# Kernel tuning notes

Hardware: AMD Instinct MI355X
Metric: run time of the kernel (lower is better)

Reference implementation:

```python
import jax, jax.numpy as jnp
import numpy as np

E = 16        # n_experts
K = 2         # n_active_experts
D = 2048      # d_model
F = 1408      # ffn_hidden
B, S = 4, 2048


def _swiglu(x, wg, wu, wd):
    # x: [N, D]; wg/wu: [F, D]; wd: [D, F]
    return (jax.nn.silu(x @ wg.T) * (x @ wu.T)) @ wd.T


def setup_inputs() -> dict:
    key = jax.random.key(0)
    ks = jax.random.split(key, 8)
    sc = 0.02
    return {
        "x": jax.random.normal(ks[0], (B, S, D), jnp.float32),
        "gate_w": jax.random.normal(ks[1], (E, D), jnp.float32) * sc,
        "w_gate": jax.random.normal(ks[2], (E, F, D), jnp.float32) * sc,
        "w_up": jax.random.normal(ks[3], (E, F, D), jnp.float32) * sc,
        "w_down": jax.random.normal(ks[4], (E, D, F), jnp.float32) * sc,
        "sw_gate": jax.random.normal(ks[5], (F, D), jnp.float32) * sc,
        "sw_up": jax.random.normal(ks[6], (F, D), jnp.float32) * sc,
        "sw_down": jax.random.normal(ks[7], (D, F), jnp.float32) * sc,
        "expert_bias": jnp.zeros((E,), jnp.float32),
    }


def reference(x, gate_w, w_gate, w_up, w_down, sw_gate, sw_up, sw_down, expert_bias):
    b, s, d = x.shape
    flat = x.reshape(-1, d)                           # [N, D]
    logits = flat @ gate_w.T                          # [N, E]
    probs = jax.nn.softmax(logits, axis=-1)
    biased = logits + expert_bias
    _, top_idx = jax.lax.top_k(biased, K)             # [N, K] int32
    top_w = jnp.take_along_axis(probs, top_idx, axis=-1)
    top_w = top_w / jnp.sum(top_w, axis=-1, keepdims=True)
    # scatter top-k weights into a dense per-expert combine matrix [N, E]
    combine = jnp.sum(jax.nn.one_hot(top_idx, E, dtype=flat.dtype) * top_w[..., None], axis=1)
    out = jnp.zeros_like(flat)
    for e in range(E):  # fixed small expert loop
        out = out + combine[:, e:e + 1] * _swiglu(flat, w_gate[e], w_up[e], w_down[e])
    out = out + _swiglu(flat, sw_gate, sw_up, sw_down)  # shared expert
    return out.reshape(b, s, d)
```

## Files before the change

kernel.cpp:

```cpp
#include <hip/hip_runtime.h>
#include <hip/hip_bf16.h>
#include <cstdint>

#define NE 16
#define D_ 2048
#define F_ 1408
#define NTOK 8192
#define NPAIR (NTOK * 2)
#define SHARED_BASE NPAIR
#define NTOT (NPAIR + NTOK)

#define BM1 256
#define BN1 128
#define BK 64
#define NF1 (F_ / BN1)
#define NF2 (D_ / BN1)
#define MAXRT1 111
#define MAXRT2 79

typedef __attribute__((ext_vector_type(8))) short short8;
typedef __attribute__((ext_vector_type(4))) float f32x4;

static __device__ __forceinline__ ushort f2bf(float f) {
    union { float f; unsigned u; } v; v.f = f;
    unsigned u = v.u;
    return (ushort)((u + 0x7FFFu + ((u >> 16) & 1u)) >> 16);
}

static __device__ __forceinline__ void cvt_store8(ushort* dst, const float* src) {
    const float4* s = reinterpret_cast<const float4*>(src);
    float4 a = s[0], b = s[1];
    short8 v;
    v[0] = (short)f2bf(a.x); v[1] = (short)f2bf(a.y);
    v[2] = (short)f2bf(a.z); v[3] = (short)f2bf(a.w);
    v[4] = (short)f2bf(b.x); v[5] = (short)f2bf(b.y);
    v[6] = (short)f2bf(b.z); v[7] = (short)f2bf(b.w);
    *reinterpret_cast<short8*>(dst) = v;
}

static __device__ __forceinline__ void gll16(const void* g, void* l) {
    __builtin_amdgcn_global_load_lds((const __attribute__((address_space(1))) void*)g,
                                     (__attribute__((address_space(3))) void*)l, 16, 0, 0);
}

__global__ __launch_bounds__(256) void k_cvt(const float* __restrict__ src,
                                             ushort* __restrict__ dst, int n8) {
    int i = blockIdx.x * 256 + threadIdx.x;
    int stride = gridDim.x * 256;
    for (; i < n8; i += stride) cvt_store8(dst + (size_t)i * 8, src + (size_t)i * 8);
}

__global__ __launch_bounds__(256) void k_route(const float* __restrict__ x,
                                               const float* __restrict__ gate_w,
                                               const float* __restrict__ expert_bias,
                                               int* __restrict__ topk_idx,
                                               float* __restrict__ topk_w) {
    const int wave = threadIdx.x >> 6;
    const int lane = threadIdx.x & 63;
    const int tok = blockIdx.x * 4 + wave;
    if (tok >= NTOK) return;
    const float* xr = x + (size_t)tok * D_;
    float xv[D_ / 64];
#pragma unroll
    for (int i = 0; i < D_ / 64; ++i) xv[i] = xr[lane + 64 * i];

    float logits[NE];
#pragma unroll
    for (int e = 0; e < NE; ++e) {
        const float* gw = gate_w + e * D_;
        float p = 0.f;
#pragma unroll
        for (int i = 0; i < D_ / 64; ++i) p += xv[i] * gw[lane + 64 * i];
#pragma unroll
        for (int off = 32; off > 0; off >>= 1) p += __shfl_xor(p, off, 64);
        logits[e] = p;
    }
    int i1 = 0; float b1 = logits[0] + expert_bias[0];
#pragma unroll
    for (int e = 1; e < NE; ++e) {
        float b = logits[e] + expert_bias[e];
        if (b > b1) { b1 = b; i1 = e; }
    }
    int i2 = -1; float b2 = -3.4e38f;
#pragma unroll
    for (int e = 0; e < NE; ++e) {
        if (e == i1) continue;
        float b = logits[e] + expert_bias[e];
        if (b > b2) { b2 = b; i2 = e; }
    }
    float l1 = logits[i1], l2 = logits[i2];
    float m = fmaxf(l1, l2);
    float e1 = __expf(l1 - m), e2 = __expf(l2 - m);
    float s = e1 + e2;
    if (lane == 0) {
        topk_idx[tok * 2 + 0] = i1;
        topk_idx[tok * 2 + 1] = i2;
        topk_w[tok * 2 + 0] = e1 / s;
        topk_w[tok * 2 + 1] = e2 / s;
    }
}

__global__ void k_zero_meta(int* meta) {
    if (threadIdx.x < 128) meta[threadIdx.x] = 0;
}

__global__ __launch_bounds__(256) void k_count(const int* __restrict__ topk_idx,
                                               int* __restrict__ meta) {
    int t = blockIdx.x * 256 + threadIdx.x;
    if (t >= NTOK) return;
    atomicAdd(&meta[topk_idx[t * 2 + 0]], 1);
    atomicAdd(&meta[topk_idx[t * 2 + 1]], 1);
}

__global__ void k_prefix(int* meta) {
    if (threadIdx.x == 0) {
        int acc = 0;
        for (int e = 0; e < NE; ++e) { meta[32 + e] = acc; acc += meta[e]; }
        meta[32 + NE] = acc;
        int t = 0;
        for (int e = 0; e < NE; ++e) { meta[64 + e] = t; t += (meta[e] + BM1 - 1) / BM1; }
        meta[64 + NE] = t;
        meta[64 + NE + 1] = t + NTOK / BM1;
    }
}

__global__ __launch_bounds__(256) void k_scatter(const int* __restrict__ topk_idx,
                                                 const float* __restrict__ topk_w,
                                                 int* __restrict__ meta,
                                                 int* __restrict__ tok_sorted,
                                                 float* __restrict__ w_sorted) {
    int t = blockIdx.x * 256 + threadIdx.x;
    if (t >= NTOK) return;
#pragma unroll
    for (int k = 0; k < 2; ++k) {
        int e = topk_idx[t * 2 + k];
        int p = atomicAdd(&meta[16 + e], 1);
        int idx = meta[32 + e] + p;
        tok_sorted[idx] = t;
        w_sorted[idx] = topk_w[t * 2 + k];
    }
}

__global__ __launch_bounds__(512, 2) void k_ffn1(const ushort* __restrict__ xb,
                                                 const ushort* __restrict__ wgb,
                                                 const ushort* __restrict__ wub,
                                                 const ushort* __restrict__ swgb,
                                                 const ushort* __restrict__ swub,
                                                 const int* __restrict__ meta,
                                                 const int* __restrict__ tok_sorted,
                                                 const float* __restrict__ w_sorted,
                                                 ushort* __restrict__ Hbuf) {
    const int bid = blockIdx.x;
    const int rt = bid / NF1;
    const int fx = bid - rt * NF1;
    if (rt >= meta[64 + NE + 1]) return;
    int e = (rt >= meta[64 + NE]) ? NE : 0;
    if (e == 0) {
#pragma unroll
        for (int i = 1; i < NE; ++i) if (rt >= meta[64 + i]) e = i;
    }
    int n_e, base;
    if (e < NE) { n_e = meta[e]; base = meta[32 + e]; }
    else        { n_e = NTOK;    base = SHARED_BASE; }
    const int row0 = (rt - meta[64 + e]) * BM1;
    const int f0 = fx * BN1;
    const ushort* wg = (e < NE) ? wgb + (size_t)e * F_ * D_ : swgb;
    const ushort* wu = (e < NE) ? wub + (size_t)e * F_ * D_ : swub;

    __shared__ __align__(16) ushort As[2][BM1 * BK];
    __shared__ __align__(16) ushort Gs[2][BN1 * BK];
    __shared__ __align__(16) ushort Us[2][BN1 * BK];
    __shared__ int tks[BM1];
    __shared__ float tws[BM1];

    const int tid = threadIdx.x;
    const int wv = tid >> 6, lane = tid & 63;
    if (tid < BM1) {
        int r = row0 + tid;
        if (r < n_e) {
            tks[tid] = (e < NE) ? tok_sorted[base + r] : r;
            tws[tid] = (e < NE) ? w_sorted[base + r] : 1.0f;
        } else { tks[tid] = 0; tws[tid] = 0.f; }
    }
    __syncthreads();

    const ushort* srcA[4]; const ushort* srcG[2]; const ushort* srcU[2];
#pragma unroll
    for (int j = 0; j < 4; ++j) {
        int c = j * 512 + wv * 64 + lane;
        int r = c >> 3;
        int col = ((c & 7) ^ (r & 7)) * 8;
        srcA[j] = xb + (size_t)tks[r] * D_ + col;
    }
#pragma unroll
    for (int j = 0; j < 2; ++j) {
        int c = j * 512 + wv * 64 + lane;
        int r = c >> 3;
        int col = ((c & 7) ^ (r & 7)) * 8;
        srcG[j] = wg + (size_t)(f0 + r) * D_ + col;
        srcU[j] = wu + (size_t)(f0 + r) * D_ + col;
    }

    auto stage = [&](int buf, int k0) {
        char* bA = (char*)(&As[buf][0]) + wv * 1024;
        char* bG = (char*)(&Gs[buf][0]) + wv * 1024;
        char* bU = (char*)(&Us[buf][0]) + wv * 1024;
        gll16(srcA[0] + k0, bA);         gll16(srcA[1] + k0, bA + 8192);
        gll16(srcA[2] + k0, bA + 16384); gll16(srcA[3] + k0, bA + 24576);
        gll16(srcG[0] + k0, bG);         gll16(srcG[1] + k0, bG + 8192);
        gll16(srcU[0] + k0, bU);         gll16(srcU[1] + k0, bU + 8192);
    };

    f32x4 accg[4][4] = {}; f32x4 accu[4][4] = {};
    const int wm = (wv >> 1) * 64, wn = (wv & 1) * 64;
    const int fr = lane & 15, fq = lane >> 4;
    const int sw = fr & 7;
    const int rc0 = ((fq ^ sw) * 8);
    const int rc1 = (((4 + fq) ^ sw) * 8);

    auto compute = [&](int buf) {
        const ushort* pA = As[buf];
        const ushort* pG = Gs[buf];
        const ushort* pU = Us[buf];
#pragma unroll
        for (int kk = 0; kk < 2; ++kk) {
            const int rc = kk ? rc1 : rc0;
            short8 af[4], gf[4], uf[4];
#pragma unroll
            for (int mi = 0; mi < 4; ++mi)
                af[mi] = *reinterpret_cast<const short8*>(&pA[(wm + mi * 16 + fr) * BK + rc]);
#pragma unroll
            for (int ni = 0; ni < 4; ++ni) {
                gf[ni] = *reinterpret_cast<const short8*>(&pG[(wn + ni * 16 + fr) * BK + rc]);
                uf[ni] = *reinterpret_cast<const short8*>(&pU[(wn + ni * 16 + fr) * BK + rc]);
            }
#pragma unroll
            for (int mi = 0; mi < 4; ++mi)
#pragma unroll
                for (int ni = 0; ni < 4; ++ni) {
                    accg[mi][ni] = __builtin_amdgcn_mfma_f32_16x16x32_bf16(af[mi], gf[ni], accg[mi][ni], 0, 0, 0);
                    accu[mi][ni] = __builtin_amdgcn_mfma_f32_16x16x32_bf16(af[mi], uf[ni], accu[mi][ni], 0, 0, 0);
                }
        }
    };

    const int NK = D_ / BK;
    stage(0, 0);
    stage(1, BK);
    asm volatile("s_waitcnt vmcnt(8)" ::: "memory");
    __builtin_amdgcn_s_barrier();
    __builtin_amdgcn_sched_barrier(0);
    int cur = 0;
    for (int ks = 0; ks < NK; ++ks) {
        compute(cur);
        __builtin_amdgcn_s_barrier();
        if (ks + 2 < NK) {
            stage(cur, (ks + 2) * BK);
            asm volatile("s_waitcnt vmcnt(8)" ::: "memory");
        } else if (ks + 1 < NK) {
            asm volatile("s_waitcnt vmcnt(0)" ::: "memory");
        }
        __builtin_amdgcn_s_barrier();
        __builtin_amdgcn_sched_barrier(0);
        cur ^= 1;
    }

#pragma unroll
    for (int mi = 0; mi < 4; ++mi) {
#pragma unroll
        for (int r = 0; r < 4; ++r) {
            int lr = wm + mi * 16 + fq * 4 + r;
            int grow = row0 + lr;
            if (grow < n_e) {
                float w = tws[lr];
                ushort* hrow = Hbuf + (size_t)(base + grow) * F_ + f0 + wn;
#pragma unroll
                for (int ni = 0; ni < 4; ++ni) {
                    float g = accg[mi][ni][r];
                    float u = accu[mi][ni][r];
                    float h = w * (g / (1.f + __expf(-g))) * u;
                    hrow[ni * 16 + fr] = f2bf(h);
                }
            }
        }
    }
}

__global__ __launch_bounds__(512, 2) void k_ffn2(const ushort* __restrict__ Hbuf,
                                                 const ushort* __restrict__ wdb,
                                                 const ushort* __restrict__ swdb,
                                                 const int* __restrict__ meta,
                                                 const int* __restrict__ tok_sorted,
                                                 float* __restrict__ out,
                                                 int shared_pass) {
    const int bid = blockIdx.x;
    const int rt = bid / NF2;
    const int dx = bid - rt * NF2;
    int e, n_e, base, row0;
    if (shared_pass) {
        e = NE; n_e = NTOK; base = SHARED_BASE; row0 = rt * BM1;
    } else {
        if (rt >= meta[64 + NE]) return;
        e = 0;
#pragma unroll
        for (int i = 1; i < NE; ++i) if (rt >= meta[64 + i]) e = i;
        n_e = meta[e]; base = meta[32 + e];
        row0 = (rt - meta[64 + e]) * BM1;
    }
    const int d0 = dx * BN1;
    const ushort* wd = (e < NE) ? wdb + (size_t)e * D_ * F_ : swdb;

    __shared__ __align__(16) ushort As[2][BM1 * BK];
    __shared__ __align__(16) ushort Bs[2][BN1 * BK];
    __shared__ int tks[BM1];

    const int tid = threadIdx.x;
    const int wv = tid >> 6, lane = tid & 63;
    if (tid < BM1) {
        int r = row0 + tid;
        tks[tid] = (r < n_e) ? ((e < NE) ? tok_sorted[base + r] : r) : -1;
    }
    __syncthreads();

    const ushort* srcA[4]; const ushort* srcB[2];
#pragma unroll
    for (int j = 0; j < 4; ++j) {
        int c = j * 512 + wv * 64 + lane;
        int r = c >> 3;
        int col = ((c & 7) ^ (r & 7)) * 8;
        srcA[j] = Hbuf + (size_t)(base + row0 + r) * F_ + col;
    }
#pragma unroll
    for (int j = 0; j < 2; ++j) {
        int c = j * 512 + wv * 64 + lane;
        int r = c >> 3;
        int col = ((c & 7) ^ (r & 7)) * 8;
        srcB[j] = wd + (size_t)(d0 + r) * F_ + col;
    }

    auto stage = [&](int buf, int k0) {
        char* bA = (char*)(&As[buf][0]) + wv * 1024;
        char* bB = (char*)(&Bs[buf][0]) + wv * 1024;
        gll16(srcA[0] + k0, bA);         gll16(srcA[1] + k0, bA + 8192);
        gll16(srcA[2] + k0, bA + 16384); gll16(srcA[3] + k0, bA + 24576);
        gll16(srcB[0] + k0, bB);         gll16(srcB[1] + k0, bB + 8192);
    };

    f32x4 acc[4][4] = {};
    const int wm = (wv >> 1) * 64, wn = (wv & 1) * 64;
    const int fr = lane & 15, fq = lane >> 4;
    const int sw = fr & 7;
    const int rc0 = ((fq ^ sw) * 8);
    const int rc1 = (((4 + fq) ^ sw) * 8);

    auto compute = [&](int buf) {
        const ushort* pA = As[buf];
        const ushort* pB = Bs[buf];
#pragma unroll
        for (int kk = 0; kk < 2; ++kk) {
            const int rc = kk ? rc1 : rc0;
            short8 af[4], bfr[4];
#pragma unroll
            for (int mi = 0; mi < 4; ++mi)
                af[mi] = *reinterpret_cast<const short8*>(&pA[(wm + mi * 16 + fr) * BK + rc]);
#pragma unroll
            for (int ni = 0; ni < 4; ++ni)
                bfr[ni] = *reinterpret_cast<const short8*>(&pB[(wn + ni * 16 + fr) * BK + rc]);
#pragma unroll
            for (int mi = 0; mi < 4; ++mi)
#pragma unroll
                for (int ni = 0; ni < 4; ++ni)
                    acc[mi][ni] = __builtin_amdgcn_mfma_f32_16x16x32_bf16(af[mi], bfr[ni], acc[mi][ni], 0, 0, 0);
        }
    };

    const int NK = F_ / BK;
    stage(0, 0);
    stage(1, BK);
    asm volatile("s_waitcnt vmcnt(6)" ::: "memory");
    __builtin_amdgcn_s_barrier();
    __builtin_amdgcn_sched_barrier(0);
    int cur = 0;
    for (int ks = 0; ks < NK; ++ks) {
        compute(cur);
        __builtin_amdgcn_s_barrier();
        if (ks + 2 < NK) {
            stage(cur, (ks + 2) * BK);
            asm volatile("s_waitcnt vmcnt(6)" ::: "memory");
        } else if (ks + 1 < NK) {
            asm volatile("s_waitcnt vmcnt(0)" ::: "memory");
        }
        __builtin_amdgcn_s_barrier();
        __builtin_amdgcn_sched_barrier(0);
        cur ^= 1;
    }

#pragma unroll
    for (int mi = 0; mi < 4; ++mi) {
#pragma unroll
        for (int r = 0; r < 4; ++r) {
            int lr = wm + mi * 16 + fq * 4 + r;
            int slot = row0 + lr;
            if (slot < n_e) {
                int t = tks[lr];
                float* orow = out + (size_t)t * D_ + d0 + wn;
#pragma unroll
                for (int ni = 0; ni < 4; ++ni) {
                    float val = acc[mi][ni][r];
                    if (shared_pass) orow[ni * 16 + fr] = val;
                    else atomicAdd(&orow[ni * 16 + fr], val);
                }
            }
        }
    }
}

extern "C" void kernel_launch(void* const* d_in, const int* in_sizes, int n_in,
                              void* d_out, int out_size, void* d_ws, size_t ws_size,
                              hipStream_t stream) {
    const float* x        = (const float*)d_in[0];
    const float* gate_w   = (const float*)d_in[1];
    const float* w_gate   = (const float*)d_in[2];
    const float* w_up     = (const float*)d_in[3];
    const float* w_down   = (const float*)d_in[4];
    const float* sw_gate  = (const float*)d_in[5];
    const float* sw_up    = (const float*)d_in[6];
    const float* sw_down  = (const float*)d_in[7];
    const float* expert_bias = (const float*)d_in[8];
    float* out = (float*)d_out;

    const size_t NW = (size_t)NE * F_ * D_;
    const size_t NSW = (size_t)F_ * D_;
    const size_t NX = (size_t)NTOK * D_;

    char* ws = (char*)d_ws;
    size_t off = 0;
    ushort* xb   = (ushort*)(ws + off); off += NX * 2;
    ushort* wgb  = (ushort*)(ws + off); off += NW * 2;
    ushort* wub  = (ushort*)(ws + off); off += NW * 2;
    ushort* wdb  = (ushort*)(ws + off); off += NW * 2;
    ushort* swgb = (ushort*)(ws + off); off += NSW * 2;
    ushort* swub = (ushort*)(ws + off); off += NSW * 2;
    ushort* swdb = (ushort*)(ws + off); off += NSW * 2;
    ushort* Hbuf = (ushort*)(ws + off); off += (size_t)NTOT * F_ * 2;
    int* tok_sorted = (int*)(ws + off); off += NPAIR * sizeof(int);
    float* w_sorted = (float*)(ws + off); off += NPAIR * sizeof(float);
    int* topk_idx = (int*)(ws + off); off += NTOK * 2 * sizeof(int);
    float* topk_w = (float*)(ws + off); off += NTOK * 2 * sizeof(float);
    int* meta = (int*)(ws + off); off += 512;

    k_route<<<NTOK / 4, 256, 0, stream>>>(x, gate_w, expert_bias, topk_idx, topk_w);
    k_zero_meta<<<1, 128, 0, stream>>>(meta);
    k_count<<<NTOK / 256, 256, 0, stream>>>(topk_idx, meta);
    k_prefix<<<1, 1, 0, stream>>>(meta);
    k_scatter<<<NTOK / 256, 256, 0, stream>>>(topk_idx, topk_w, meta, tok_sorted, w_sorted);

    auto cvt = [&](const float* s, ushort* d, size_t n) {
        int n8 = (int)(n / 8);
        int blocks = (n8 + 255) / 256;
        if (blocks > 4096) blocks = 4096;
        k_cvt<<<blocks, 256, 0, stream>>>(s, d, n8);
    };
    cvt(x, xb, NX);
    cvt(w_gate, wgb, NW);
    cvt(w_up, wub, NW);
    cvt(w_down, wdb, NW);
    cvt(sw_gate, swgb, NSW);
    cvt(sw_up, swub, NSW);
    cvt(sw_down, swdb, NSW);

    k_ffn1<<<MAXRT1 * NF1, 512, 0, stream>>>(xb, wgb, wub, swgb, swub,
                                             meta, tok_sorted, w_sorted, Hbuf);

    k_ffn2<<<(NTOK / BM1) * NF2, 512, 0, stream>>>(Hbuf, wdb, swdb, meta, tok_sorted, out, 1);
    k_ffn2<<<MAXRT2 * NF2, 512, 0, stream>>>(Hbuf, wdb, swdb, meta, tok_sorted, out, 0);
}
```

Measured before the change: 974.5 us.

## Interleave LDS reads and MFMA phases with barriers and priority boosts in FFN GEMMs

Splits each K-step of both grouped GEMM kernels into alternating LDS-fragment-load and MFMA phases separated by workgroup barriers. MFMA phases run under raised wave priority (s_setprio), a ping-pong schedule meant to let waves overlap one another's memory and matrix work. In the first kernel the A/G prefetch for step k+2 now issues before the last up-projection MFMA block, so global loads overlap compute. The cost is many extra barriers per iteration, which could stall the waves. The vmcnt accounting also becomes fragile: the wait count is unchanged even though loads are now issued in two groups.

```diff
diff --git a/kernel.cpp b/kernel.cpp
--- a/kernel.cpp
+++ b/kernel.cpp
@@ -140,6 +140,8 @@
         w_sorted[idx] = topk_w[t * 2 + k];
     }
 }
+
+#define LD8(P, ROW, RC) (*reinterpret_cast<const short8*>(&(P)[(ROW) * BK + (RC)]))
 
 __global__ __launch_bounds__(512, 2) void k_ffn1(const ushort* __restrict__ xb,
                                                  const ushort* __restrict__ wgb,
@@ -201,13 +203,15 @@
         srcU[j] = wu + (size_t)(f0 + r) * D_ + col;
     }
 
-    auto stage = [&](int buf, int k0) {
+    auto stageAG = [&](int buf, int k0) {
         char* bA = (char*)(&As[buf][0]) + wv * 1024;
         char* bG = (char*)(&Gs[buf][0]) + wv * 1024;
-        char* bU = (char*)(&Us[buf][0]) + wv * 1024;
         gll16(srcA[0] + k0, bA);         gll16(srcA[1] + k0, bA + 8192);
         gll16(srcA[2] + k0, bA + 16384); gll16(srcA[3] + k0, bA + 24576);
         gll16(srcG[0] + k0, bG);         gll16(srcG[1] + k0, bG + 8192);
+    };
+    auto stageU = [&](int buf, int k0) {
+        char* bU = (char*)(&Us[buf][0]) + wv * 1024;
         gll16(srcU[0] + k0, bU);         gll16(srcU[1] + k0, bU + 8192);
     };
 
@@ -218,51 +222,83 @@
     const int rc0 = ((fq ^ sw) * 8);
     const int rc1 = (((4 + fq) ^ sw) * 8);
 
-    auto compute = [&](int buf) {
-        const ushort* pA = As[buf];
-        const ushort* pG = Gs[buf];
-        const ushort* pU = Us[buf];
-#pragma unroll
-        for (int kk = 0; kk < 2; ++kk) {
-            const int rc = kk ? rc1 : rc0;
-            short8 af[4], gf[4], uf[4];
-#pragma unroll
-            for (int mi = 0; mi < 4; ++mi)
-                af[mi] = *reinterpret_cast<const short8*>(&pA[(wm + mi * 16 + fr) * BK + rc]);
-#pragma unroll
-            for (int ni = 0; ni < 4; ++ni) {
-                gf[ni] = *reinterpret_cast<const short8*>(&pG[(wn + ni * 16 + fr) * BK + rc]);
-                uf[ni] = *reinterpret_cast<const short8*>(&pU[(wn + ni * 16 + fr) * BK + rc]);
-            }
-#pragma unroll
-            for (int mi = 0; mi < 4; ++mi)
-#pragma unroll
-                for (int ni = 0; ni < 4; ++ni) {
-                    accg[mi][ni] = __builtin_amdgcn_mfma_f32_16x16x32_bf16(af[mi], gf[ni], accg[mi][ni], 0, 0, 0);
-                    accu[mi][ni] = __builtin_amdgcn_mfma_f32_16x16x32_bf16(af[mi], uf[ni], accu[mi][ni], 0, 0, 0);
-                }
-        }
-    };
-
     const int NK = D_ / BK;
-    stage(0, 0);
-    stage(1, BK);
+    stageAG(0, 0); stageU(0, 0);
+    stageAG(1, BK); stageU(1, BK);
     asm volatile("s_waitcnt vmcnt(8)" ::: "memory");
     __builtin_amdgcn_s_barrier();
     __builtin_amdgcn_sched_barrier(0);
-    int cur = 0;
+
     for (int ks = 0; ks < NK; ++ks) {
-        compute(cur);
-        __builtin_amdgcn_s_barrier();
-        if (ks + 2 < NK) {
-            stage(cur, (ks + 2) * BK);
+        const int cur = ks & 1;
+        const ushort* pA = As[cur];
+        const ushort* pG = Gs[cur];
+        const ushort* pU = Us[cur];
+        const bool st = (ks + 2 < NK);
+        const int k2 = (ks + 2) * BK;
+        short8 af[4], gf[4], uf[4];
+
+#pragma unroll
+        for (int mi = 0; mi < 4; ++mi) af[mi] = LD8(pA, wm + mi * 16 + fr, rc0);
+#pragma unroll
+        for (int ni = 0; ni < 4; ++ni) gf[ni] = LD8(pG, wn + ni * 16 + fr, rc0);
+        __builtin_amdgcn_s_barrier();
+        __builtin_amdgcn_s_setprio(1);
+#pragma unroll
+        for (int mi = 0; mi < 4; ++mi)
+#pragma unroll
+            for (int ni = 0; ni < 4; ++ni)
+                accg[mi][ni] = __builtin_amdgcn_mfma_f32_16x16x32_bf16(af[mi], gf[ni], accg[mi][ni], 0, 0, 0);
+        __builtin_amdgcn_s_setprio(0);
+        __builtin_amdgcn_s_barrier();
+
+#pragma unroll
+        for (int ni = 0; ni < 4; ++ni) uf[ni] = LD8(pU, wn + ni * 16 + fr, rc0);
+        __builtin_amdgcn_s_barrier();
+        __builtin_amdgcn_s_setprio(1);
+#pragma unroll
+        for (int mi = 0; mi < 4; ++mi)
+#pragma unroll
+            for (int ni = 0; ni < 4; ++ni)
+                accu[mi][ni] = __builtin_amdgcn_mfma_f32_16x16x32_bf16(af[mi], uf[ni], accu[mi][ni], 0, 0, 0);
+        __builtin_amdgcn_s_setprio(0);
+        __builtin_amdgcn_s_barrier();
+
+#pragma unroll
+        for (int mi = 0; mi < 4; ++mi) af[mi] = LD8(pA, wm + mi * 16 + fr, rc1);
+#pragma unroll
+        for (int ni = 0; ni < 4; ++ni) gf[ni] = LD8(pG, wn + ni * 16 + fr, rc1);
+        __builtin_amdgcn_s_barrier();
+        __builtin_amdgcn_s_setprio(1);
+#pragma unroll
+        for (int mi = 0; mi < 4; ++mi)
+#pragma unroll
+            for (int ni = 0; ni < 4; ++ni)
+                accg[mi][ni] = __builtin_amdgcn_mfma_f32_16x16x32_bf16(af[mi], gf[ni], accg[mi][ni], 0, 0, 0);
+        __builtin_amdgcn_s_setprio(0);
+        __builtin_amdgcn_s_barrier();
+
+#pragma unroll
+        for (int ni = 0; ni < 4; ++ni) uf[ni] = LD8(pU, wn + ni * 16 + fr, rc1);
+        if (st) stageAG(cur, k2);
+        __builtin_amdgcn_s_barrier();
+        __builtin_amdgcn_s_setprio(1);
+#pragma unroll
+        for (int mi = 0; mi < 4; ++mi)
+#pragma unroll
+            for (int ni = 0; ni < 4; ++ni)
+                accu[mi][ni] = __builtin_amdgcn_mfma_f32_16x16x32_bf16(af[mi], uf[ni], accu[mi][ni], 0, 0, 0);
+        __builtin_amdgcn_s_setprio(0);
+        __builtin_amdgcn_s_barrier();
+
+        if (st) {
+            stageU(cur, k2);
             asm volatile("s_waitcnt vmcnt(8)" ::: "memory");
         } else if (ks + 1 < NK) {
             asm volatile("s_waitcnt vmcnt(0)" ::: "memory");
         }
         __builtin_amdgcn_s_barrier();
         __builtin_amdgcn_sched_barrier(0);
-        cur ^= 1;
     }
 
 #pragma unroll
@@ -353,38 +389,49 @@
     const int rc0 = ((fq ^ sw) * 8);
     const int rc1 = (((4 + fq) ^ sw) * 8);
 
-    auto compute = [&](int buf) {
-        const ushort* pA = As[buf];
-        const ushort* pB = Bs[buf];
-#pragma unroll
-        for (int kk = 0; kk < 2; ++kk) {
-            const int rc = kk ? rc1 : rc0;
-            short8 af[4], bfr[4];
-#pragma unroll
-            for (int mi = 0; mi < 4; ++mi)
-                af[mi] = *reinterpret_cast<const short8*>(&pA[(wm + mi * 16 + fr) * BK + rc]);
-#pragma unroll
-            for (int ni = 0; ni < 4; ++ni)
-                bfr[ni] = *reinterpret_cast<const short8*>(&pB[(wn + ni * 16 + fr) * BK + rc]);
-#pragma unroll
-            for (int mi = 0; mi < 4; ++mi)
-#pragma unroll
-                for (int ni = 0; ni < 4; ++ni)
-                    acc[mi][ni] = __builtin_amdgcn_mfma_f32_16x16x32_bf16(af[mi], bfr[ni], acc[mi][ni], 0, 0, 0);
-        }
-    };
-
     const int NK = F_ / BK;
     stage(0, 0);
     stage(1, BK);
     asm volatile("s_waitcnt vmcnt(6)" ::: "memory");
     __builtin_amdgcn_s_barrier();
     __builtin_amdgcn_sched_barrier(0);
-    int cur = 0;
+
     for (int ks = 0; ks < NK; ++ks) {
-        compute(cur);
-        __builtin_amdgcn_s_barrier();
-        if (ks + 2 < NK) {
+        const int cur = ks & 1;
+        const ushort* pA = As[cur];
+        const ushort* pB = Bs[cur];
+        const bool st = (ks + 2 < NK);
+        short8 af[4], bfr[4];
+
+#pragma unroll
+        for (int mi = 0; mi < 4; ++mi) af[mi] = LD8(pA, wm + mi * 16 + fr, rc0);
+#pragma unroll
+        for (int ni = 0; ni < 4; ++ni) bfr[ni] = LD8(pB, wn + ni * 16 + fr, rc0);
+        __builtin_amdgcn_s_barrier();
+        __builtin_amdgcn_s_setprio(1);
+#pragma unroll
+        for (int mi = 0; mi < 4; ++mi)
+#pragma unroll
+            for (int ni = 0; ni < 4; ++ni)
+                acc[mi][ni] = __builtin_amdgcn_mfma_f32_16x16x32_bf16(af[mi], bfr[ni], acc[mi][ni], 0, 0, 0);
+        __builtin_amdgcn_s_setprio(0);
+        __builtin_amdgcn_s_barrier();
+
+#pragma unroll
+        for (int mi = 0; mi < 4; ++mi) af[mi] = LD8(pA, wm + mi * 16 + fr, rc1);
+#pragma unroll
+        for (int ni = 0; ni < 4; ++ni) bfr[ni] = LD8(pB, wn + ni * 16 + fr, rc1);
+        __builtin_amdgcn_s_barrier();
+        __builtin_amdgcn_s_setprio(1);
+#pragma unroll
+        for (int mi = 0; mi < 4; ++mi)
+#pragma unroll
+            for (int ni = 0; ni < 4; ++ni)
+                acc[mi][ni] = __builtin_amdgcn_mfma_f32_16x16x32_bf16(af[mi], bfr[ni], acc[mi][ni], 0, 0, 0);
+        __builtin_amdgcn_s_setprio(0);
+        __builtin_amdgcn_s_barrier();
+
+        if (st) {
             stage(cur, (ks + 2) * BK);
             asm volatile("s_waitcnt vmcnt(6)" ::: "memory");
         } else if (ks + 1 < NK) {
@@ -392,7 +439,6 @@
         }
         __builtin_amdgcn_s_barrier();
         __builtin_amdgcn_sched_barrier(0);
-        cur ^= 1;
     }
 
 #pragma unroll
```

New measurement: 1.065 ms. 1.09x slower.

## Replace atomic scatter in down-projection with bf16 staging buffer and gather

Applied to the files above, without the earlier changes.

The down-projection now runs routed and shared tiles in a single launch. It writes per-slot bf16 results into a staging buffer that reuses the expert gate-weight workspace, instead of storing and atomically adding fp32 values into the output. A new gather kernel uses an inverse index from the scatter step to sum each token's two expert rows and its shared row into fp32 output. This removes fp32 atomics and the second launch. In exchange it adds an extra read and write pass and rounds partial results to bf16 before summation.

```diff
diff --git a/kernel.cpp b/kernel.cpp
--- a/kernel.cpp
+++ b/kernel.cpp
@@ -15,8 +15,7 @@
 #define BK 64
 #define NF1 (F_ / BN1)
 #define NF2 (D_ / BN1)
-#define MAXRT1 111
-#define MAXRT2 79
+#define MAXRT 111
 
 typedef __attribute__((ext_vector_type(8))) short short8;
 typedef __attribute__((ext_vector_type(4))) float f32x4;
@@ -25,6 +24,11 @@
     union { float f; unsigned u; } v; v.f = f;
     unsigned u = v.u;
     return (ushort)((u + 0x7FFFu + ((u >> 16) & 1u)) >> 16);
+}
+
+static __device__ __forceinline__ float bf2f(ushort u) {
+    union { unsigned u; float f; } v; v.u = ((unsigned)u) << 16;
+    return v.f;
 }
 
 static __device__ __forceinline__ void cvt_store8(ushort* dst, const float* src) {
@@ -128,7 +132,8 @@
                                                  const float* __restrict__ topk_w,
                                                  int* __restrict__ meta,
                                                  int* __restrict__ tok_sorted,
-                                                 float* __restrict__ w_sorted) {
+                                                 float* __restrict__ w_sorted,
+                                                 int* __restrict__ inv) {
     int t = blockIdx.x * 256 + threadIdx.x;
     if (t >= NTOK) return;
 #pragma unroll
@@ -138,6 +143,7 @@
         int idx = meta[32 + e] + p;
         tok_sorted[idx] = t;
         w_sorted[idx] = topk_w[t * 2 + k];
+        inv[t * 2 + k] = idx;
     }
 }
 
@@ -290,37 +296,28 @@
                                                  const ushort* __restrict__ wdb,
                                                  const ushort* __restrict__ swdb,
                                                  const int* __restrict__ meta,
-                                                 const int* __restrict__ tok_sorted,
-                                                 float* __restrict__ out,
-                                                 int shared_pass) {
+                                                 ushort* __restrict__ Obuf) {
     const int bid = blockIdx.x;
     const int rt = bid / NF2;
     const int dx = bid - rt * NF2;
-    int e, n_e, base, row0;
-    if (shared_pass) {
-        e = NE; n_e = NTOK; base = SHARED_BASE; row0 = rt * BM1;
-    } else {
-        if (rt >= meta[64 + NE]) return;
-        e = 0;
+    if (rt >= meta[64 + NE + 1]) return;
+    int e = (rt >= meta[64 + NE]) ? NE : 0;
+    if (e == 0) {
 #pragma unroll
         for (int i = 1; i < NE; ++i) if (rt >= meta[64 + i]) e = i;
-        n_e = meta[e]; base = meta[32 + e];
-        row0 = (rt - meta[64 + e]) * BM1;
-    }
+    }
+    int n_e, base;
+    if (e < NE) { n_e = meta[e]; base = meta[32 + e]; }
+    else        { n_e = NTOK;    base = SHARED_BASE; }
+    const int row0 = (rt - meta[64 + e]) * BM1;
     const int d0 = dx * BN1;
     const ushort* wd = (e < NE) ? wdb + (size_t)e * D_ * F_ : swdb;
 
     __shared__ __align__(16) ushort As[2][BM1 * BK];
     __shared__ __align__(16) ushort Bs[2][BN1 * BK];
-    __shared__ int tks[BM1];
 
     const int tid = threadIdx.x;
     const int wv = tid >> 6, lane = tid & 63;
-    if (tid < BM1) {
-        int r = row0 + tid;
-        tks[tid] = (r < n_e) ? ((e < NE) ? tok_sorted[base + r] : r) : -1;
-    }
-    __syncthreads();
 
     const ushort* srcA[4]; const ushort* srcB[2];
 #pragma unroll
@@ -402,17 +399,36 @@
             int lr = wm + mi * 16 + fq * 4 + r;
             int slot = row0 + lr;
             if (slot < n_e) {
-                int t = tks[lr];
-                float* orow = out + (size_t)t * D_ + d0 + wn;
-#pragma unroll
-                for (int ni = 0; ni < 4; ++ni) {
-                    float val = acc[mi][ni][r];
-                    if (shared_pass) orow[ni * 16 + fr] = val;
-                    else atomicAdd(&orow[ni * 16 + fr], val);
-                }
+                ushort* orow = Obuf + (size_t)(base + slot) * D_ + d0 + wn;
+#pragma unroll
+                for (int ni = 0; ni < 4; ++ni)
+                    orow[ni * 16 + fr] = f2bf(acc[mi][ni][r]);
             }
         }
     }
+}
+
+__global__ __launch_bounds__(256) void k_gather(const ushort* __restrict__ Obuf,
+                                                const int* __restrict__ inv,
+                                                float* __restrict__ out) {
+    const int t = blockIdx.x;
+    const int c = threadIdx.x * 8;
+    const int s1 = inv[t * 2 + 0];
+    const int s2 = inv[t * 2 + 1];
+    short8 a = *reinterpret_cast<const short8*>(&Obuf[(size_t)s1 * D_ + c]);
+    short8 b = *reinterpret_cast<const short8*>(&Obuf[(size_t)s2 * D_ + c]);
+    short8 d = *reinterpret_cast<const short8*>(&Obuf[(size_t)(SHARED_BASE + t) * D_ + c]);
+    float4 o0, o1;
+    o0.x = bf2f((ushort)a[0]) + bf2f((ushort)b[0]) + bf2f((ushort)d[0]);
+    o0.y = bf2f((ushort)a[1]) + bf2f((ushort)b[1]) + bf2f((ushort)d[1]);
+    o0.z = bf2f((ushort)a[2]) + bf2f((ushort)b[2]) + bf2f((ushort)d[2]);
+    o0.w = bf2f((ushort)a[3]) + bf2f((ushort)b[3]) + bf2f((ushort)d[3]);
+    o1.x = bf2f((ushort)a[4]) + bf2f((ushort)b[4]) + bf2f((ushort)d[4]);
+    o1.y = bf2f((ushort)a[5]) + bf2f((ushort)b[5]) + bf2f((ushort)d[5]);
+    o1.z = bf2f((ushort)a[6]) + bf2f((ushort)b[6]) + bf2f((ushort)d[6]);
+    o1.w = bf2f((ushort)a[7]) + bf2f((ushort)b[7]) + bf2f((ushort)d[7]);
+    float4* op = reinterpret_cast<float4*>(out + (size_t)t * D_ + c);
+    op[0] = o0; op[1] = o1;
 }
 
 extern "C" void kernel_launch(void* const* d_in, const int* in_sizes, int n_in,
@@ -447,13 +463,16 @@
     float* w_sorted = (float*)(ws + off); off += NPAIR * sizeof(float);
     int* topk_idx = (int*)(ws + off); off += NTOK * 2 * sizeof(int);
     float* topk_w = (float*)(ws + off); off += NTOK * 2 * sizeof(float);
+    int* inv = (int*)(ws + off); off += NTOK * 2 * sizeof(int);
     int* meta = (int*)(ws + off); off += 512;
+
+    ushort* Obuf = wgb;
 
     k_route<<<NTOK / 4, 256, 0, stream>>>(x, gate_w, expert_bias, topk_idx, topk_w);
     k_zero_meta<<<1, 128, 0, stream>>>(meta);
     k_count<<<NTOK / 256, 256, 0, stream>>>(topk_idx, meta);
     k_prefix<<<1, 1, 0, stream>>>(meta);
-    k_scatter<<<NTOK / 256, 256, 0, stream>>>(topk_idx, topk_w, meta, tok_sorted, w_sorted);
+    k_scatter<<<NTOK / 256, 256, 0, stream>>>(topk_idx, topk_w, meta, tok_sorted, w_sorted, inv);
 
     auto cvt = [&](const float* s, ushort* d, size_t n) {
         int n8 = (int)(n / 8);
@@ -469,9 +488,10 @@
     cvt(sw_up, swub, NSW);
     cvt(sw_down, swdb, NSW);
 
-    k_ffn1<<<MAXRT1 * NF1, 512, 0, stream>>>(xb, wgb, wub, swgb, swub,
-                                             meta, tok_sorted, w_sorted, Hbuf);
-
-    k_ffn2<<<(NTOK / BM1) * NF2, 512, 0, stream>>>(Hbuf, wdb, swdb, meta, tok_sorted, out, 1);
-    k_ffn2<<<MAXRT2 * NF2, 512, 0, stream>>>(Hbuf, wdb, swdb, meta, tok_sorted, out, 0);
-}
+    k_ffn1<<<MAXRT * NF1, 512, 0, stream>>>(xb, wgb, wub, swgb, swub,
+                                            meta, tok_sorted, w_sorted, Hbuf);
+
+    k_ffn2<<<MAXRT * NF2, 512, 0, stream>>>(Hbuf, wdb, swdb, meta, Obuf);
+
+    k_gather<<<NTOK, 256, 0, stream>>>(Obuf, inv, out);
+}
```

Result: faster. 949.8 us (-2.5%).
